# Kernel tuning notes

Measured on AMD Instinct MI355X. Metric: run time of the kernel, lower is better.

The kernel has to match this reference:

```python
import jax, jax.numpy as jnp
import numpy as np

B, L, D = 2, 2048, 1024
H, DK, DV = 16, 64, 64
EPS = 1e-6


def setup_inputs() -> dict:
    key = jax.random.key(0)
    ks = jax.random.split(key, 7)
    s = 0.02
    return {
        "x": jax.random.normal(ks[0], (B, L, D), dtype=jnp.float32),
        "Wq": jax.random.normal(ks[1], (D, H * DK), dtype=jnp.float32) * s,
        "Wk": jax.random.normal(ks[2], (D, H * DK), dtype=jnp.float32) * s,
        "Wv": jax.random.normal(ks[3], (D, H * DV), dtype=jnp.float32) * s,
        "Wo": jax.random.normal(ks[4], (H * DV, D), dtype=jnp.float32) * s,
        "ln_gamma": jnp.ones((D,), dtype=jnp.float32),
        "ln_beta": jnp.zeros((D,), dtype=jnp.float32),
    }


def reference(x, Wq, Wk, Wv, Wo, ln_gamma, ln_beta):
    temp = jnp.asarray(DK, x.dtype) ** 0.5
    # projections -> [B, H, L, Dh]
    q = (x @ Wq).reshape(B, L, H, DK).transpose(0, 2, 1, 3)
    k = (x @ Wk).reshape(B, L, H, DK).transpose(0, 2, 1, 3)
    v = (x @ Wv).reshape(B, L, H, DV).transpose(0, 2, 1, 3)
    # naive attention: explicit [B,H,L,L] scores (dropout rate 0 -> identity)
    scores = jnp.einsum("bhqd,bhkd->bhqk", q / temp, k)
    attn = jax.nn.softmax(scores, axis=-1)
    o = jnp.einsum("bhqk,bhkd->bhqd", attn, v)
    o = o.transpose(0, 2, 1, 3).reshape(B, L, H * DV)
    out = o @ Wo + x  # residual
    # LayerNorm(eps=1e-6)
    mu = jnp.mean(out, axis=-1, keepdims=True)
    var = jnp.var(out, axis=-1, keepdims=True)
    return (out - mu) * jax.lax.rsqrt(var + EPS) * ln_gamma + ln_beta
```

## Files before the change

kernel.cpp:

```cpp
#include <hip/hip_runtime.h>


typedef __bf16 bf16;
typedef __bf16 bf16x2 __attribute__((ext_vector_type(2)));
typedef __bf16 bf16x4 __attribute__((ext_vector_type(4)));
typedef __bf16 bf16x8 __attribute__((ext_vector_type(8)));
typedef float floatx4 __attribute__((ext_vector_type(4)));
typedef int intx4 __attribute__((ext_vector_type(4)));

#define MFMA16(a, b, c) __builtin_amdgcn_mfma_f32_16x16x32_bf16((a), (b), (c), 0, 0, 0)

__device__ __forceinline__ void gll16(const bf16* g, bf16* l) {
  __builtin_amdgcn_global_load_lds((const __attribute__((address_space(1))) void*)g,
                                   (__attribute__((address_space(3))) void*)l, 16, 0, 0);
}

__global__ __launch_bounds__(256) void k_prep_x(const float* __restrict__ x, bf16* __restrict__ xb) {
  const int i = (blockIdx.x * 256 + threadIdx.x) * 4;
  const float4 v = *reinterpret_cast<const float4*>(x + i);
  bf16x4 o = {(bf16)v.x, (bf16)v.y, (bf16)v.z, (bf16)v.w};
  *reinterpret_cast<bf16x4*>(xb + i) = o;
}

__global__ __launch_bounds__(256) void k_prep_w(const float* __restrict__ Wq, const float* __restrict__ Wk,
                                                const float* __restrict__ Wv, const float* __restrict__ Wo,
                                                bf16* __restrict__ WT) {
  __shared__ float tile[32][33];
  const int z = blockIdx.z;
  const float* W = (z == 0) ? Wq : (z == 1) ? Wk : (z == 2) ? Wv : Wo;
  const int n0 = blockIdx.x * 32, k0 = blockIdx.y * 32;
  const int tx = threadIdx.x, ty = threadIdx.y;
#pragma unroll
  for (int j = 0; j < 32; j += 8)
    tile[ty + j][tx] = W[(size_t)(k0 + ty + j) * 1024 + n0 + tx];
  __syncthreads();
#pragma unroll
  for (int j = 0; j < 32; j += 8)
    WT[(size_t)(z * 1024 + n0 + ty + j) * 1024 + k0 + tx] = (bf16)tile[tx][ty + j];
}

template <int MODE>
__global__ __launch_bounds__(256) void k_gemm(const bf16* __restrict__ A, const bf16* __restrict__ Bt,
                                              const float* __restrict__ X, float* __restrict__ Y,
                                              bf16* __restrict__ QB, bf16* __restrict__ KB,
                                              bf16* __restrict__ VTB) {
  __shared__ __align__(16) bf16 As[128 * 64];
  __shared__ __align__(16) bf16 Bs[128 * 64];
  const int t = threadIdx.x;
  const int lane = t & 63, wv = t >> 6;
  const int qd = lane >> 4, col = lane & 15;
  const int c7 = col & 7;
  const int wm = wv >> 1, wn = wv & 1;
  const int m0 = blockIdx.x * 128, n0 = blockIdx.y * 128;
  const int srow = wv * 8 + (lane >> 3);
  const int scol = ((lane & 7) ^ (lane >> 3)) * 8;
  const bf16* Ag = A + (size_t)(m0 + srow) * 1024 + scol;
  const bf16* Bg = Bt + (size_t)(n0 + srow) * 1024 + scol;

  floatx4 acc[4][4] = {};

  for (int kt = 0; kt < 1024; kt += 64) {
    __syncthreads();
#pragma unroll
    for (int rd = 0; rd < 4; rd++) {
      gll16(Ag + (size_t)rd * 32 * 1024 + kt, As + (rd * 32 + wv * 8) * 64);
      gll16(Bg + (size_t)rd * 32 * 1024 + kt, Bs + (rd * 32 + wv * 8) * 64);
    }
    __syncthreads();
#pragma unroll
    for (int ks = 0; ks < 2; ks++) {
      bf16x8 af[4], bfr[4];
#pragma unroll
      for (int i = 0; i < 4; i++)
        af[i] = *reinterpret_cast<const bf16x8*>(As + (wm * 64 + i * 16 + col) * 64 + ((ks * 4 + qd) ^ c7) * 8);
#pragma unroll
      for (int i = 0; i < 4; i++)
        bfr[i] = *reinterpret_cast<const bf16x8*>(Bs + (wn * 64 + i * 16 + col) * 64 + ((ks * 4 + qd) ^ c7) * 8);
#pragma unroll
      for (int i = 0; i < 4; i++)
#pragma unroll
        for (int j = 0; j < 4; j++)
          acc[i][j] = MFMA16(af[i], bfr[j], acc[i][j]);
    }
  }

#pragma unroll
  for (int i = 0; i < 4; i++) {
#pragma unroll
    for (int j = 0; j < 4; j++) {
      const int mb = m0 + wm * 64 + i * 16 + qd * 4;
      const int n = n0 + wn * 64 + j * 16 + col;
      if (MODE == 0) {
        const int seg = n >> 10;
        const int h = (n & 1023) >> 6, dd = n & 63;
#pragma unroll
        for (int r = 0; r < 4; r++) {
          const int m = mb + r;
          const int bb = m >> 11, l = m & 2047;
          const float v = acc[i][j][r];
          if (seg == 0)
            QB[((size_t)(bb * 16 + h) * 2048 + l) * 64 + dd] = (bf16)(v * 0.18033688f);
          else if (seg == 1)
            KB[((size_t)(bb * 16 + h) * 2048 + l) * 64 + dd] = (bf16)v;
          else
            VTB[((size_t)(bb * 16 + h) * 64 + dd) * 2048 + l] = (bf16)v;
        }
      } else {
#pragma unroll
        for (int r = 0; r < 4; r++) {
          const int m = mb + r;
          Y[(size_t)m * 1024 + n] = acc[i][j][r] + X[(size_t)m * 1024 + n];
        }
      }
    }
  }
}

__global__ __launch_bounds__(256) void k_attn(const bf16* __restrict__ QB, const bf16* __restrict__ KB,
                                              const bf16* __restrict__ VTB, bf16* __restrict__ OB) {
  __shared__ __align__(16) bf16 Ks0[64 * 64];
  __shared__ __align__(16) bf16 Vs0[64 * 64];
  __shared__ __align__(16) bf16 Ks1[64 * 64];
  __shared__ __align__(16) bf16 Vs1[64 * 64];
  const int t = threadIdx.x;
  const int lane = t & 63, wv = t >> 6;
  const int qd = lane >> 4, col = lane & 15;
  const int c7 = col & 7;
  const int bh = blockIdx.y;
  const int qr = blockIdx.x * 128 + wv * 32;
  const int lrow0 = wv * 8 + (lane >> 3);
  const int swz = ((lane & 7) ^ (lane >> 3)) * 8;
  const int kg0 = ((lrow0 >> 5) << 5) + (((lrow0 >> 2) & 3) << 3) + (((lrow0 >> 4) & 1) << 2) + (lrow0 & 3);
  const int r1 = lrow0 + 32;
  const int kg1 = ((r1 >> 5) << 5) + (((r1 >> 2) & 3) << 3) + (((r1 >> 4) & 1) << 2) + (r1 & 3);
  const bf16* Kg0 = KB + ((size_t)bh * 2048 + kg0) * 64 + swz;
  const bf16* Kg1 = KB + ((size_t)bh * 2048 + kg1) * 64 + swz;
  const bf16* Vg0 = VTB + ((size_t)bh * 64 + lrow0) * 2048 + swz;
  const bf16* Vg1 = VTB + ((size_t)bh * 64 + lrow0 + 32) * 2048 + swz;

  bf16x8 bQ[2][2];
#pragma unroll
  for (int qt = 0; qt < 2; qt++)
#pragma unroll
    for (int s = 0; s < 2; s++)
      bQ[qt][s] = *reinterpret_cast<const bf16x8*>(QB + ((size_t)bh * 2048 + qr + qt * 16 + col) * 64 + s * 32 + qd * 8);

  floatx4 oacc[2][4] = {};
  float lsum[2] = {0.f, 0.f};
  floatx4 scur[2][4];
  int pk[2][4][2];

#define STAGE_TO(KD, VD, i)                               \
  do {                                                    \
    gll16(Kg0 + (size_t)(i) * 4096, KD + (wv * 8) * 64);  \
    gll16(Kg1 + (size_t)(i) * 4096, KD + (32 + wv * 8) * 64); \
    gll16(Vg0 + (i) * 64, VD + (wv * 8) * 64);            \
    gll16(Vg1 + (i) * 64, VD + (32 + wv * 8) * 64);       \
  } while (0)

#define QK_FROM(ks_)                                                                                  \
  do {                                                                                                \
    _Pragma("unroll") for (int nt = 0; nt < 4; nt++) {                                                \
      bf16x8 a0 = *reinterpret_cast<const bf16x8*>(ks_ + (nt * 16 + col) * 64 + (qd ^ c7) * 8);       \
      bf16x8 a1 = *reinterpret_cast<const bf16x8*>(ks_ + (nt * 16 + col) * 64 + ((4 + qd) ^ c7) * 8); \
      _Pragma("unroll") for (int qt = 0; qt < 2; qt++) {                                              \
        floatx4 z = {0.f, 0.f, 0.f, 0.f};                                                             \
        z = MFMA16(a0, bQ[qt][0], z);                                                                 \
        z = MFMA16(a1, bQ[qt][1], z);                                                                 \
        scur[qt][nt] = z;                                                                             \
      }                                                                                               \
    }                                                                                                 \
  } while (0)

#define EXPPACK()                                                                               \
  do {                                                                                          \
    _Pragma("unroll") for (int qt = 0; qt < 2; qt++) {                                          \
      _Pragma("unroll") for (int nt = 0; nt < 4; nt++) {                                        \
        const float e0 = exp2f(scur[qt][nt][0]), e1 = exp2f(scur[qt][nt][1]);                   \
        const float e2 = exp2f(scur[qt][nt][2]), e3 = exp2f(scur[qt][nt][3]);                   \
        lsum[qt] += (e0 + e1) + (e2 + e3);                                                      \
        bf16x2 p01, p23;                                                                        \
        p01[0] = (bf16)e0; p01[1] = (bf16)e1;                                                   \
        p23[0] = (bf16)e2; p23[1] = (bf16)e3;                                                   \
        pk[qt][nt][0] = __builtin_bit_cast(int, p01);                                           \
        pk[qt][nt][1] = __builtin_bit_cast(int, p23);                                           \
      }                                                                                         \
    }                                                                                           \
  } while (0)

#define PV_FROM(vs_)                                                                                  \
  do {                                                                                                \
    bf16x8 bV[4][2];                                                                                  \
    _Pragma("unroll") for (int nd = 0; nd < 4; nd++) {                                                \
      bV[nd][0] = *reinterpret_cast<const bf16x8*>(vs_ + (nd * 16 + col) * 64 + (qd ^ c7) * 8);       \
      bV[nd][1] = *reinterpret_cast<const bf16x8*>(vs_ + (nd * 16 + col) * 64 + ((4 + qd) ^ c7) * 8); \
    }                                                                                                 \
    _Pragma("unroll") for (int qt = 0; qt < 2; qt++) {                                                \
      _Pragma("unroll") for (int s = 0; s < 2; s++) {                                                 \
        intx4 w;                                                                                      \
        w[0] = pk[qt][2 * s][0]; w[1] = pk[qt][2 * s][1];                                             \
        w[2] = pk[qt][2 * s + 1][0]; w[3] = pk[qt][2 * s + 1][1];                                     \
        const bf16x8 aP = __builtin_bit_cast(bf16x8, w);                                              \
        _Pragma("unroll") for (int nd = 0; nd < 4; nd++)                                              \
          oacc[qt][nd] = MFMA16(aP, bV[nd][s], oacc[qt][nd]);                                         \
      }                                                                                               \
    }                                                                                                 \
  } while (0)

  STAGE_TO(Ks0, Vs0, 0);
  __syncthreads();
  for (int ii = 0; ii < 16; ii++) {
    const int i1 = 2 * ii + 1;
    STAGE_TO(Ks1, Vs1, i1);
    QK_FROM(Ks0);
    EXPPACK();
    PV_FROM(Vs0);
    __syncthreads();
    if (i1 < 31) STAGE_TO(Ks0, Vs0, i1 + 1);
    QK_FROM(Ks1);
    EXPPACK();
    PV_FROM(Vs1);
    __syncthreads();
  }

#pragma unroll
  for (int qt = 0; qt < 2; qt++) {
    lsum[qt] += __shfl_xor(lsum[qt], 16);
    lsum[qt] += __shfl_xor(lsum[qt], 32);
  }
  const int bb = bh >> 4, h = bh & 15;
#pragma unroll
  for (int qt = 0; qt < 2; qt++) {
#pragma unroll
    for (int r = 0; r < 4; r++) {
      const float linv = 1.f / __shfl(lsum[qt], qd * 4 + r);
      const size_t m = (size_t)bb * 2048 + qr + qt * 16 + qd * 4 + r;
#pragma unroll
      for (int nd = 0; nd < 4; nd++)
        OB[m * 1024 + h * 64 + nd * 16 + col] = (bf16)(oacc[qt][nd][r] * linv);
    }
  }
#undef STAGE_TO
#undef QK_FROM
#undef EXPPACK
#undef PV_FROM
}

__global__ __launch_bounds__(256) void k_ln(const float* __restrict__ Yin, const float* __restrict__ gamma,
                                            const float* __restrict__ beta, float* __restrict__ out) {
  __shared__ float red[8];
  const int row = blockIdx.x, t = threadIdx.x;
  const float4 v = *reinterpret_cast<const float4*>(Yin + (size_t)row * 1024 + t * 4);
  float s = v.x + v.y + v.z + v.w;
  float ss = v.x * v.x + v.y * v.y + v.z * v.z + v.w * v.w;
#pragma unroll
  for (int d = 1; d < 64; d <<= 1) {
    s += __shfl_xor(s, d);
    ss += __shfl_xor(ss, d);
  }
  if ((t & 63) == 0) {
    red[t >> 6] = s;
    red[4 + (t >> 6)] = ss;
  }
  __syncthreads();
  s = red[0] + red[1] + red[2] + red[3];
  ss = red[4] + red[5] + red[6] + red[7];
  const float mu = s * (1.f / 1024.f);
  const float var = ss * (1.f / 1024.f) - mu * mu;
  const float rs = rsqrtf(var + 1e-6f);
  const float4 g = *reinterpret_cast<const float4*>(gamma + t * 4);
  const float4 bt = *reinterpret_cast<const float4*>(beta + t * 4);
  float4 o;
  o.x = (v.x - mu) * rs * g.x + bt.x;
  o.y = (v.y - mu) * rs * g.y + bt.y;
  o.z = (v.z - mu) * rs * g.z + bt.z;
  o.w = (v.w - mu) * rs * g.w + bt.w;
  *reinterpret_cast<float4*>(out + (size_t)row * 1024 + t * 4) = o;
}

extern "C" void kernel_launch(void* const* d_in, const int* in_sizes, int n_in,
                              void* d_out, int out_size, void* d_ws, size_t ws_size,
                              hipStream_t stream) {
  (void)in_sizes; (void)n_in; (void)out_size; (void)ws_size;
  const float* x = (const float*)d_in[0];
  const float* Wq = (const float*)d_in[1];
  const float* Wk = (const float*)d_in[2];
  const float* Wv = (const float*)d_in[3];
  const float* Wo = (const float*)d_in[4];
  const float* gamma = (const float*)d_in[5];
  const float* beta = (const float*)d_in[6];

  char* ws = (char*)d_ws;
  const size_t MB = 1ull << 20;
  bf16* XB = (bf16*)(ws);
  bf16* OB = (bf16*)(ws);
  bf16* WT = (bf16*)(ws + 8 * MB);
  bf16* QB = (bf16*)(ws + 16 * MB);
  bf16* KB = (bf16*)(ws + 24 * MB);
  bf16* VTB = (bf16*)(ws + 32 * MB);
  float* Y = (float*)(ws + 16 * MB);

  k_prep_x<<<4096, 256, 0, stream>>>(x, XB);
  k_prep_w<<<dim3(32, 32, 4), dim3(32, 8), 0, stream>>>(Wq, Wk, Wv, Wo, WT);
  k_gemm<0><<<dim3(32, 24), 256, 0, stream>>>(XB, WT, nullptr, nullptr, QB, KB, VTB);
  k_attn<<<dim3(16, 32), 256, 0, stream>>>(QB, KB, VTB, OB);
  k_gemm<1><<<dim3(32, 8), 256, 0, stream>>>(OB, WT + (size_t)3072 * 1024, x, Y,
                                             nullptr, nullptr, nullptr);
  k_ln<<<4096, 256, 0, stream>>>(Y, gamma, beta, (float*)d_out);
}
```

Baseline: 216.0 us.

## Split attention KV range across two wave groups and software-pipeline QK with PV

The attention block grows to 512 threads. Two groups of four waves each handle half of the key/value sequence for the same 128 query rows, and their partial outputs and row sums are combined through shared memory at the end. The main loop is also restructured so that QK for the next tile is issued while the exp/pack and PV of the previous tile proceed, with staging interleaved. This aims to raise the number of waves per query tile and to overlap MFMA work with LDS loads, at the cost of doubled LDS use, an extra reduction pass and more barriers.

```diff
diff --git a/kernel.cpp b/kernel.cpp
--- a/kernel.cpp
+++ b/kernel.cpp
@@ -116,19 +116,19 @@
   }
 }
 
-__global__ __launch_bounds__(256) void k_attn(const bf16* __restrict__ QB, const bf16* __restrict__ KB,
+__global__ __launch_bounds__(512) void k_attn(const bf16* __restrict__ QB, const bf16* __restrict__ KB,
                                               const bf16* __restrict__ VTB, bf16* __restrict__ OB) {
-  __shared__ __align__(16) bf16 Ks0[64 * 64];
-  __shared__ __align__(16) bf16 Vs0[64 * 64];
-  __shared__ __align__(16) bf16 Ks1[64 * 64];
-  __shared__ __align__(16) bf16 Vs1[64 * 64];
+  __shared__ __align__(16) bf16 smem[2][4][64 * 64];
+  __shared__ float LL[128];
   const int t = threadIdx.x;
   const int lane = t & 63, wv = t >> 6;
+  const int wq = wv & 3, half = wv >> 2;
   const int qd = lane >> 4, col = lane & 15;
   const int c7 = col & 7;
   const int bh = blockIdx.y;
-  const int qr = blockIdx.x * 128 + wv * 32;
-  const int lrow0 = wv * 8 + (lane >> 3);
+  const int qr = blockIdx.x * 128 + wq * 32;
+  const int kb = half * 16;
+  const int lrow0 = wq * 8 + (lane >> 3);
   const int swz = ((lane & 7) ^ (lane >> 3)) * 8;
   const int kg0 = ((lrow0 >> 5) << 5) + (((lrow0 >> 2) & 3) << 3) + (((lrow0 >> 4) & 1) << 2) + (lrow0 & 3);
   const int r1 = lrow0 + 32;
@@ -150,16 +150,20 @@
   floatx4 scur[2][4];
   int pk[2][4][2];
 
-#define STAGE_TO(KD, VD, i)                               \
-  do {                                                    \
-    gll16(Kg0 + (size_t)(i) * 4096, KD + (wv * 8) * 64);  \
-    gll16(Kg1 + (size_t)(i) * 4096, KD + (32 + wv * 8) * 64); \
-    gll16(Vg0 + (i) * 64, VD + (wv * 8) * 64);            \
-    gll16(Vg1 + (i) * 64, VD + (32 + wv * 8) * 64);       \
+#define STAGE(j)                                                             \
+  do {                                                                       \
+    bf16* kd_ = &smem[half][((j)&1) * 2][0];                                 \
+    bf16* vd_ = &smem[half][((j)&1) * 2 + 1][0];                             \
+    const size_t i_ = kb + (j);                                              \
+    gll16(Kg0 + i_ * 4096, kd_ + (wq * 8) * 64);                             \
+    gll16(Kg1 + i_ * 4096, kd_ + (32 + wq * 8) * 64);                        \
+    gll16(Vg0 + i_ * 64, vd_ + (wq * 8) * 64);                               \
+    gll16(Vg1 + i_ * 64, vd_ + (32 + wq * 8) * 64);                          \
   } while (0)
 
-#define QK_FROM(ks_)                                                                                  \
+#define QK(j)                                                                                         \
   do {                                                                                                \
+    const bf16* ks_ = &smem[half][((j)&1) * 2][0];                                                    \
     _Pragma("unroll") for (int nt = 0; nt < 4; nt++) {                                                \
       bf16x8 a0 = *reinterpret_cast<const bf16x8*>(ks_ + (nt * 16 + col) * 64 + (qd ^ c7) * 8);       \
       bf16x8 a1 = *reinterpret_cast<const bf16x8*>(ks_ + (nt * 16 + col) * 64 + ((4 + qd) ^ c7) * 8); \
@@ -188,8 +192,9 @@
     }                                                                                           \
   } while (0)
 
-#define PV_FROM(vs_)                                                                                  \
+#define PV(j)                                                                                         \
   do {                                                                                                \
+    const bf16* vs_ = &smem[half][((j)&1) * 2 + 1][0];                                                \
     bf16x8 bV[4][2];                                                                                  \
     _Pragma("unroll") for (int nd = 0; nd < 4; nd++) {                                                \
       bV[nd][0] = *reinterpret_cast<const bf16x8*>(vs_ + (nd * 16 + col) * 64 + (qd ^ c7) * 8);       \
@@ -207,43 +212,63 @@
     }                                                                                                 \
   } while (0)
 
-  STAGE_TO(Ks0, Vs0, 0);
-  __syncthreads();
-  for (int ii = 0; ii < 16; ii++) {
-    const int i1 = 2 * ii + 1;
-    STAGE_TO(Ks1, Vs1, i1);
-    QK_FROM(Ks0);
+  STAGE(0);
+  __syncthreads();
+  QK(0);
+  for (int j = 1; j < 16; j++) {
+    __syncthreads();
+    STAGE(j);
     EXPPACK();
-    PV_FROM(Vs0);
+    PV(j - 1);
     __syncthreads();
-    if (i1 < 31) STAGE_TO(Ks0, Vs0, i1 + 1);
-    QK_FROM(Ks1);
-    EXPPACK();
-    PV_FROM(Vs1);
-    __syncthreads();
-  }
+    QK(j);
+  }
+  EXPPACK();
+  PV(15);
 
 #pragma unroll
   for (int qt = 0; qt < 2; qt++) {
     lsum[qt] += __shfl_xor(lsum[qt], 16);
     lsum[qt] += __shfl_xor(lsum[qt], 32);
   }
-  const int bb = bh >> 4, h = bh & 15;
-#pragma unroll
-  for (int qt = 0; qt < 2; qt++) {
-#pragma unroll
-    for (int r = 0; r < 4; r++) {
-      const float linv = 1.f / __shfl(lsum[qt], qd * 4 + r);
-      const size_t m = (size_t)bb * 2048 + qr + qt * 16 + qd * 4 + r;
+
+  float* LO = reinterpret_cast<float*>(&smem[0][0][0]);
+  __syncthreads();
+  if (half == 1) {
+#pragma unroll
+    for (int qt = 0; qt < 2; qt++)
 #pragma unroll
       for (int nd = 0; nd < 4; nd++)
-        OB[m * 1024 + h * 64 + nd * 16 + col] = (bf16)(oacc[qt][nd][r] * linv);
-    }
-  }
-#undef STAGE_TO
-#undef QK_FROM
+#pragma unroll
+        for (int r = 0; r < 4; r++)
+          LO[(wq * 32 + qt * 16 + qd * 4 + r) * 64 + nd * 16 + col] = oacc[qt][nd][r];
+    if (qd == 0) {
+#pragma unroll
+      for (int qt = 0; qt < 2; qt++) LL[wq * 32 + qt * 16 + col] = lsum[qt];
+    }
+  }
+  __syncthreads();
+  if (half == 0) {
+    const int bb = bh >> 4, h = bh & 15;
+#pragma unroll
+    for (int qt = 0; qt < 2; qt++) {
+      const float ltot = lsum[qt] + LL[wq * 32 + qt * 16 + col];
+#pragma unroll
+      for (int r = 0; r < 4; r++) {
+        const float linv = 1.f / __shfl(ltot, qd * 4 + r);
+        const size_t m = (size_t)bb * 2048 + qr + qt * 16 + qd * 4 + r;
+#pragma unroll
+        for (int nd = 0; nd < 4; nd++) {
+          const float o1 = LO[(wq * 32 + qt * 16 + qd * 4 + r) * 64 + nd * 16 + col];
+          OB[m * 1024 + h * 64 + nd * 16 + col] = (bf16)((oacc[qt][nd][r] + o1) * linv);
+        }
+      }
+    }
+  }
+#undef STAGE
+#undef QK
 #undef EXPPACK
-#undef PV_FROM
+#undef PV
 }
 
 __global__ __launch_bounds__(256) void k_ln(const float* __restrict__ Yin, const float* __restrict__ gamma,
@@ -303,7 +328,7 @@
   k_prep_x<<<4096, 256, 0, stream>>>(x, XB);
   k_prep_w<<<dim3(32, 32, 4), dim3(32, 8), 0, stream>>>(Wq, Wk, Wv, Wo, WT);
   k_gemm<0><<<dim3(32, 24), 256, 0, stream>>>(XB, WT, nullptr, nullptr, QB, KB, VTB);
-  k_attn<<<dim3(16, 32), 256, 0, stream>>>(QB, KB, VTB, OB);
+  k_attn<<<dim3(16, 32), 512, 0, stream>>>(QB, KB, VTB, OB);
   k_gemm<1><<<dim3(32, 8), 256, 0, stream>>>(OB, WT + (size_t)3072 * 1024, x, Y,
                                              nullptr, nullptr, nullptr);
   k_ln<<<4096, 256, 0, stream>>>(Y, gamma, beta, (float*)d_out);
```

Result: faster. 211.0 us (-2.3%).
